# Performance work log

Measured on AMD Instinct MI355X. Metric: run time of the kernel, lower is better.

Reference implementation:

```python
import jax, jax.numpy as jnp
import numpy as np

B, N, D, E, F, K = 2, 2048, 768, 8, 3072, 2
V_MAX = 3.0
FEAT_CLAMP = 10.0


def setup_inputs() -> dict:
    key = jax.random.key(0)
    ks = jax.random.split(key, 8)
    s = lambda k, shape, sc: (jax.random.normal(k, shape, jnp.float32) * sc)
    return {
        "x": s(ks[0], (B, N, D), 1.0),
        "v_w": s(ks[1], (D,), 0.02),
        "v_b": jnp.zeros((), jnp.float32),
        "gate_w": s(ks[2], (D, E), 0.02),
        "gate_b": jnp.zeros((E,), jnp.float32),
        "w1": s(ks[3], (E, D, F), 0.02),
        "b1": jnp.zeros((E, F), jnp.float32),
        "w2": s(ks[4], (E, F, D), 0.02),
        "b2": jnp.zeros((E, D), jnp.float32),
        "out_w": s(ks[5], (2, D), 0.02),
        "out_b": jnp.zeros((D,), jnp.float32),
        "bk_scale": jnp.ones((D,), jnp.float32),
    }


def bk_green_diag(a):
    # a: (B, N) complex64 diagonal of (H_eps - z), unit off-diagonals.
    # Stable two-sided continued-fraction (Thomas/LDU) recursion:
    #   d_i = a_i - 1/d_{i-1},  e_i = a_i - 1/e_{i+1},  G_ii = 1/(d_i + e_i - a_i)
    aT = jnp.swapaxes(a, 0, 1)  # (N, B)

    def step(c, ai):
        d = ai - 1.0 / c
        return d, d

    d0 = aT[0]
    _, d_rest = jax.lax.scan(step, d0, aT[1:])
    d = jnp.concatenate([d0[None], d_rest], axis=0)  # (N, B)

    eN = aT[-1]
    _, e_rest = jax.lax.scan(step, eN, aT[:-1], reverse=True)
    e = jnp.concatenate([e_rest, eN[None]], axis=0)  # (N, B)

    G = 1.0 / (d + e - aT)
    return jnp.swapaxes(G, 0, 1)  # (B, N) complex


def reference(x, v_w, v_b, gate_w, gate_b, w1, b1, w2, b2, out_w, out_b, bk_scale):
    # --- potential projection: v = clamp(Linear(x), +-3) ---
    v = jnp.clip(x @ v_w + v_b, -V_MAX, V_MAX)  # (B, N)
    # H_eps diagonal = -2 + v, z = 1j  ->  A = H_eps - z
    a = ((-2.0 + v).astype(jnp.complex64) - 1j)
    G = bk_green_diag(a)  # (B, N) complex
    feats = jnp.stack([G.real, G.imag], axis=-1)  # (B, N, 2)

    # --- sparse MoE FFN (top-k softmax gating, GELU experts) ---
    logits = x @ gate_w + gate_b  # (B, N, E)
    probs = jax.nn.softmax(logits, axis=-1)
    topv, topi = jax.lax.top_k(probs, K)
    topv = topv / jnp.sum(topv, axis=-1, keepdims=True)
    comb = jnp.sum(topv[..., None] * jax.nn.one_hot(topi, E, dtype=x.dtype), axis=2)  # (B, N, E)
    h = jax.nn.gelu(jnp.einsum("bnd,edf->bnef", x, w1) + b1)  # (B, N, E, F)
    y = jnp.einsum("bnef,efd->bned", h, w2) + b2  # (B, N, E, D)
    ffn_out = jnp.einsum("bne,bned->bnd", comb, y)

    # --- spectral branch: clamp features, project to d_model, scale ---
    feats_c = jnp.clip(feats, -FEAT_CLAMP, FEAT_CLAMP)
    spec_out = feats_c @ out_w + out_b  # (B, N, D)
    return ffn_out + bk_scale * spec_out
```

## Files before the change

### kernel.cpp

```cpp
#include <hip/hip_runtime.h>
#include <hip/hip_bf16.h>

#define BB 2
#define NN 2048
#define DD 768
#define EE 8
#define FF 3072
#define TOK (BB*NN)
#define ROWS_CAP 9216
#define TILES 72

typedef __attribute__((ext_vector_type(8))) __bf16 bf16x8;
typedef __attribute__((ext_vector_type(4))) float floatx4;

#define OFF_CTRL    0ull
#define OFF_V       1024ull
#define OFF_TOKE    17408ull
#define OFF_TOKW    50176ull
#define OFF_ROWTOK  82944ull
#define OFF_ROWW    119808ull
#define OFF_SLOT    156672ull
#define OFF_FEATS   189440ull
#define OFF_W2T     222208ull
#define OFF_XBF     37970944ull
#define OFF_W1T     44262400ull
#define OFF_H       82011136ull
#define OFF_Y       OFF_XBF

__device__ __forceinline__ ushort f2b(float f) {
    union { float f; unsigned int i; } v; v.f = f;
    unsigned int u = v.i;
    unsigned int r = (u + 0x7FFFu + ((u >> 16) & 1u)) >> 16;
    return (ushort)r;
}
__device__ __forceinline__ unsigned int pk2(float lo, float hi) {
    union { float f; unsigned int u; } a, b;
    a.f = lo; b.f = hi;
    unsigned int ra = ((a.u + 0x7FFFu + ((a.u >> 16) & 1u)) >> 16) & 0xFFFFu;
    unsigned int rb = (b.u + 0x7FFFu + ((b.u >> 16) & 1u)) & 0xFFFF0000u;
    return ra | rb;
}
__device__ __forceinline__ float gelu_f(float x) {
    float z = 0.7978845608028654f * x * (1.f + 0.044715f * x * x);
    z = fminf(fmaxf(z, -12.f), 12.f);
    float e = __expf(2.f * z);
    return 0.5f * x * (1.f + (e - 1.f) / (e + 1.f));
}
__device__ __forceinline__ void gload16(const ushort* g, ushort* l) {
    __builtin_amdgcn_global_load_lds((const __attribute__((address_space(1))) void*)g,
                                     (__attribute__((address_space(3))) void*)l,
                                     16, 0, 0);
}

struct cplx { float x, y; };
__device__ __forceinline__ cplx cmulc(cplx a, cplx b) { return {a.x*b.x - a.y*b.y, a.x*b.y + a.y*b.x}; }
__device__ __forceinline__ cplx caddc(cplx a, cplx b) { return {a.x + b.x, a.y + b.y}; }
__device__ __forceinline__ cplx cdivc(cplx a, cplx b) {
    float s = 1.f / (b.x*b.x + b.y*b.y);
    return {(a.x*b.x + a.y*b.y)*s, (a.y*b.x - a.x*b.y)*s};
}
struct mob { cplx m00, m01, m10, m11; };
__device__ __forceinline__ mob mmul(const mob& A, const mob& B) {
    mob C;
    C.m00 = caddc(cmulc(A.m00, B.m00), cmulc(A.m01, B.m10));
    C.m01 = caddc(cmulc(A.m00, B.m01), cmulc(A.m01, B.m11));
    C.m10 = caddc(cmulc(A.m10, B.m00), cmulc(A.m11, B.m10));
    C.m11 = caddc(cmulc(A.m10, B.m01), cmulc(A.m11, B.m11));
    return C;
}
__device__ __forceinline__ void mnorm(mob& A) {
    float s = fabsf(A.m00.x);
    s = fmaxf(s, fabsf(A.m00.y)); s = fmaxf(s, fabsf(A.m01.x)); s = fmaxf(s, fabsf(A.m01.y));
    s = fmaxf(s, fabsf(A.m10.x)); s = fmaxf(s, fabsf(A.m10.y)); s = fmaxf(s, fabsf(A.m11.x));
    s = fmaxf(s, fabsf(A.m11.y));
    float r = 1.f / fmaxf(s, 1e-30f);
    A.m00.x *= r; A.m00.y *= r; A.m01.x *= r; A.m01.y *= r;
    A.m10.x *= r; A.m10.y *= r; A.m11.x *= r; A.m11.y *= r;
}
__device__ __forceinline__ mob mstep(cplx a, const mob& P) {
    mob C;
    C.m00 = {a.x*P.m00.x - a.y*P.m00.y - P.m10.x, a.x*P.m00.y + a.y*P.m00.x - P.m10.y};
    C.m01 = {a.x*P.m01.x - a.y*P.m01.y - P.m11.x, a.x*P.m01.y + a.y*P.m01.x - P.m11.y};
    C.m10 = P.m00; C.m11 = P.m01;
    return C;
}
__device__ __forceinline__ void mstore(float* s, const mob& A) {
    s[0]=A.m00.x; s[1]=A.m00.y; s[2]=A.m01.x; s[3]=A.m01.y;
    s[4]=A.m10.x; s[5]=A.m10.y; s[6]=A.m11.x; s[7]=A.m11.y;
}
__device__ __forceinline__ mob mload(const float* s) {
    mob A;
    A.m00 = {s[0], s[1]}; A.m01 = {s[2], s[3]};
    A.m10 = {s[4], s[5]}; A.m11 = {s[6], s[7]};
    return A;
}

template<bool PERM>
__device__ __forceinline__ void tcvt64_body(
    const float* __restrict__ src, ushort* __restrict__ dst,
    int Rs, int Cs, int r0, int c0, ushort* __restrict__ tT , int tid)
{
    int lr = tid >> 2;
    int lc0 = (tid & 3) * 16;
    const float* sp = src + (size_t)(r0 + lr) * Cs + c0 + lc0;
    float4 v[4];
    #pragma unroll
    for (int u = 0; u < 4; u++) v[u] = *(const float4*)(sp + 4*u);
    #pragma unroll
    for (int u = 0; u < 4; u++) {
        tT[(lc0 + 4*u + 0) * 72 + lr] = f2b(v[u].x);
        tT[(lc0 + 4*u + 1) * 72 + lr] = f2b(v[u].y);
        tT[(lc0 + 4*u + 2) * 72 + lr] = f2b(v[u].z);
        tT[(lc0 + 4*u + 3) * 72 + lr] = f2b(v[u].w);
    }
    __syncthreads();
    int chunk = tid & 7;
    #pragma unroll
    for (int pass = 0; pass < 2; pass++) {
        int c = (tid >> 3) + pass * 32;
        size_t off = (size_t)(c0 + c) * Rs + r0 + chunk * 8;
        if (PERM) {
            int a64 = chunk * 8;
            int g32 = (a64 >> 5) * 32;
            int a = a64 & 31;
            ushort o8[8] __attribute__((aligned(16)));
            #pragma unroll
            for (int k = 0; k < 8; k++) {
                int pk = a + k;
                int rl = g32 + (pk >> 1) + ((pk & 1) << 4);
                o8[k] = tT[c * 72 + rl];
            }
            *(uint4*)(dst + off) = *(const uint4*)o8;
        } else {
            *(uint4*)(dst + off) = *(const uint4*)(tT + c * 72 + chunk * 8);
        }
    }
}

#define NB_CVT   ((TOK*DD)/8/256)
#define NB_ROUTE (TOK/4)
#define NB_W1T   (12*48*EE)

__device__ __forceinline__ void cvt_body(const float* __restrict__ src, ushort* __restrict__ dst, int i) {
    const float4* s = ((const float4*)src) + (size_t)i * 2;
    float4 a = s[0], b = s[1];
    uint4 o;
    o.x = pk2(a.x, a.y); o.y = pk2(a.z, a.w);
    o.z = pk2(b.x, b.y); o.w = pk2(b.z, b.w);
    *(((uint4*)dst) + i) = o;
}

__device__ __forceinline__ void routing_body(
    const float* __restrict__ x, const float* __restrict__ v_w, const float* __restrict__ v_b,
    const float* __restrict__ gate_w, const float* __restrict__ gate_b,
    float* __restrict__ v_out, int* __restrict__ tok_e, float* __restrict__ tok_w, int blk)
{
    int wave = threadIdx.x >> 6, lane = threadIdx.x & 63;
    int t = blk * 4 + wave;
    const float* xr = x + (size_t)t * DD;
    float av = 0.f;
    float ag[8] = {0.f, 0.f, 0.f, 0.f, 0.f, 0.f, 0.f, 0.f};
    #pragma unroll
    for (int i = 0; i < 12; i++) {
        int d = lane + 64 * i;
        float xv = xr[d];
        av += xv * v_w[d];
        const float4* g = (const float4*)(gate_w + d * 8);
        float4 g0 = g[0], g1 = g[1];
        ag[0] += xv * g0.x; ag[1] += xv * g0.y; ag[2] += xv * g0.z; ag[3] += xv * g0.w;
        ag[4] += xv * g1.x; ag[5] += xv * g1.y; ag[6] += xv * g1.z; ag[7] += xv * g1.w;
    }
    #pragma unroll
    for (int off = 32; off >= 1; off >>= 1) {
        av += __shfl_xor(av, off);
        #pragma unroll
        for (int e = 0; e < 8; e++) ag[e] += __shfl_xor(ag[e], off);
    }
    if (lane == 0) {
        float vv = av + v_b[0];
        vv = fminf(fmaxf(vv, -3.f), 3.f);
        v_out[t] = vv;
        float lg[8];
        #pragma unroll
        for (int e = 0; e < 8; e++) lg[e] = ag[e] + gate_b[e];
        int e0 = 0;
        #pragma unroll
        for (int e = 1; e < 8; e++) if (lg[e] > lg[e0]) e0 = e;
        int e1 = -1;
        #pragma unroll
        for (int e = 0; e < 8; e++) if (e != e0 && (e1 < 0 || lg[e] > lg[e1])) e1 = e;
        float w0 = 1.f / (1.f + __expf(lg[e1] - lg[e0]));
        tok_e[2*t] = e0; tok_e[2*t+1] = e1;
        tok_w[2*t] = w0; tok_w[2*t+1] = 1.f - w0;
    }
}

__global__ __launch_bounds__(256) void prep1_kernel(
    const float* __restrict__ x, ushort* __restrict__ x_bf,
    const float* __restrict__ v_w, const float* __restrict__ v_b,
    const float* __restrict__ gate_w, const float* __restrict__ gate_b,
    float* __restrict__ v_out, int* __restrict__ tok_e, float* __restrict__ tok_w,
    const float* __restrict__ w1, ushort* __restrict__ w1t)
{
    __shared__ __align__(16) ushort tT[64 * 72];
    int id = blockIdx.x;
    if (id < NB_CVT) {
        cvt_body(x, x_bf, id * 256 + threadIdx.x);
        return;
    }
    id -= NB_CVT;
    if (id < NB_ROUTE) {
        routing_body(x, v_w, v_b, gate_w, gate_b, v_out, tok_e, tok_w, id);
        return;
    }
    id -= NB_ROUTE;
    int e = id / (12 * 48);
    int rem = id - e * 12 * 48;
    int cy = rem / 12;
    int rx = rem - cy * 12;
    tcvt64_body<false>(w1 + (size_t)e * DD * FF, w1t + (size_t)e * FF * DD,
                       DD, FF, rx * 64, cy * 64, tT, threadIdx.x);
}

__device__ void setup_body(
    const int* __restrict__ tok_e, const float* __restrict__ tok_w,
    int* __restrict__ ctrl, int* __restrict__ row_token, float* __restrict__ row_w,
    int* __restrict__ slot)
{
    __shared__ int cnt[8], base[8], cursor[8];
    int tid = threadIdx.x;
    int lane = tid & 63;
    if (tid < 8) { cnt[tid] = 0; cursor[tid] = 0; }
    __syncthreads();

    int mye[8];
    #pragma unroll
    for (int it = 0; it < 8; it++) {
        int idx = it * 1024 + tid;
        int e = tok_e[idx];
        mye[it] = e;
        #pragma unroll
        for (int ex = 0; ex < 8; ex++) {
            unsigned long long m = __ballot(e == ex);
            if (e == ex && lane == (__ffsll((long long)m) - 1))
                atomicAdd(&cnt[ex], (int)__popcll(m));
        }
    }
    __syncthreads();
    if (tid == 0) {
        int b = 0;
        int* te = ctrl + 24;
        for (int i = 0; i < TILES; i++) te[i] = -1;
        #pragma unroll
        for (int e = 0; e < EE; e++) {
            base[e] = b;
            ctrl[16 + e] = b;
            int tiles = (cnt[e] + 127) >> 7;
            int t0 = b >> 7;
            for (int i = 0; i < tiles; i++) te[t0 + i] = e;
            b += tiles << 7;
        }
    }
    for (int p = tid; p < ROWS_CAP; p += 1024) row_token[p] = -1;
    __syncthreads();

    #pragma unroll
    for (int it = 0; it < 8; it++) {
        int idx = it * 1024 + tid;
        int e = mye[it];
        unsigned long long lt = (1ull << lane) - 1ull;
        int p = 0;
        #pragma unroll
        for (int ex = 0; ex < 8; ex++) {
            unsigned long long m = __ballot(e == ex);
            if (e == ex) {
                int leader = __ffsll((long long)m) - 1;
                int pos = (int)__popcll(m & lt);
                int bp = 0;
                if (lane == leader) bp = atomicAdd(&cursor[ex], (int)__popcll(m));
                bp = __shfl(bp, leader);
                p = base[ex] + bp + pos;
            }
        }
        row_token[p] = idx >> 1;
        row_w[p] = tok_w[idx];
        slot[idx] = p;
    }
}

__device__ void bk_body(int b, const float* __restrict__ v, float* __restrict__ feats) {
    int t = threadIdx.x;
    bool act = t < 256;
    __shared__ float sm[256][8];
    const mob I = {{1.f,0.f},{0.f,0.f},{0.f,0.f},{1.f,0.f}};
    cplx a[8];
    const float* vb = v + (size_t)b * NN;
    if (act) {
        #pragma unroll
        for (int j = 0; j < 8; j++) { a[j].x = -2.f + vb[t*8 + j]; a[j].y = -1.f; }
    }

    mob cur = I;
    if (act) {
        #pragma unroll
        for (int j = 0; j < 8; j++) cur = mstep(a[j], cur);
        mnorm(cur);
        mstore(sm[t], cur);
    }
    for (int s = 1; s < 256; s <<= 1) {
        __syncthreads();
        mob prev; bool has = act && (t >= s);
        if (has) prev = mload(sm[t - s]);
        __syncthreads();
        if (has) { cur = mmul(cur, prev); mnorm(cur); mstore(sm[t], cur); }
    }
    __syncthreads();
    cplx dreg[8];
    if (act) {
        mob P = (t > 0) ? mload(sm[t - 1]) : I;
        #pragma unroll
        for (int j = 0; j < 8; j++) {
            P = mstep(a[j], P); mnorm(P);
            dreg[j] = cdivc(P.m00, P.m10);
        }
    }
    __syncthreads();

    cur = I;
    if (act) {
        #pragma unroll
        for (int j = 7; j >= 0; j--) cur = mstep(a[j], cur);
        mnorm(cur);
        mstore(sm[t], cur);
    }
    for (int s = 1; s < 256; s <<= 1) {
        __syncthreads();
        mob nxt; bool has = act && (t + s < 256);
        if (has) nxt = mload(sm[t + s]);
        __syncthreads();
        if (has) { cur = mmul(cur, nxt); mnorm(cur); mstore(sm[t], cur); }
    }
    __syncthreads();
    if (act) {
        mob P = (t < 255) ? mload(sm[t + 1]) : I;
        #pragma unroll
        for (int j = 7; j >= 0; j--) {
            P = mstep(a[j], P); mnorm(P);
            cplx e = cdivc(P.m00, P.m10);
            cplx den = {dreg[j].x + e.x - a[j].x, dreg[j].y + e.y - a[j].y};
            cplx one = {1.f, 0.f};
            cplx G = cdivc(one, den);
            int i = b * NN + t*8 + j;
            feats[2*i]   = G.x;
            feats[2*i+1] = G.y;
        }
    }
}

__global__ __launch_bounds__(1024) void setup_bk_kernel(
    const int* __restrict__ tok_e, const float* __restrict__ tok_w,
    int* __restrict__ ctrl, int* __restrict__ row_token, float* __restrict__ row_w,
    int* __restrict__ slot, const float* __restrict__ v, float* __restrict__ feats)
{
    if (blockIdx.x == 0) setup_body(tok_e, tok_w, ctrl, row_token, row_w, slot);
    else                 bk_body(blockIdx.x - 1, v, feats);
}

#define MFMAS() do { \
        _Pragma("unroll") \
        for (int i = 0; i < 4; i++) \
            _Pragma("unroll") \
            for (int j = 0; j < 4; j++) \
                acc[i][j] = __builtin_amdgcn_mfma_f32_16x16x32_bf16(afr[i], bfr[j], acc[i][j], 0, 0, 0); \
    } while (0)

#define G1N   (24 * 36)
#define NW2T  (48 * 12 * EE / 2)

__global__ __launch_bounds__(512, 4) void gemm1_fused_kernel(
    const ushort* __restrict__ x_bf, const ushort* __restrict__ w1t, const float* __restrict__ b1,
    const int* __restrict__ ctrl, const int* __restrict__ row_token, ushort* __restrict__ H,
    const float* __restrict__ w2, ushort* __restrict__ w2t)
{
    __shared__ __align__(16) ushort SH[4][256 * 32];
    __shared__ int toks[256];
    int bid = blockIdx.x;
    int tid = threadIdx.x;

    if (bid >= G1N) {
        int tt = (bid - G1N) * 2 + (tid >> 8);
        int e = tt / (48 * 12);
        int rem = tt - e * 48 * 12;
        int cy = rem / 48;
        int rx = rem - cy * 48;
        ushort* tT = &SH[0][0] + (tid >> 8) * 4608;
        tcvt64_body<true>(w2 + (size_t)e * FF * DD, w2t + (size_t)e * DD * FF,
                          FF, DD, rx * 64, cy * 64, tT, tid & 255);
        return;
    }

    int fx = bid % 24;
    int tile = bid / 24;
    int e0 = ctrl[24 + 2*tile];
    if (e0 < 0) return;
    int e1 = ctrl[24 + 2*tile + 1];
    if (e1 < 0) e1 = e0;
    int p0 = tile * 256;
    int f0 = fx * 128;

    ushort* As0 = &SH[0][0];
    ushort* As1 = &SH[1][0];
    ushort* Bs0 = &SH[2][0];
    ushort* Bs1 = &SH[3][0];

    if (tid < 256) { int tk = row_token[p0 + tid]; toks[tid] = tk < 0 ? 0 : tk; }
    __syncthreads();

    int wave = tid >> 6, lane = tid & 63;
    int rsub = lane >> 2;
    int kq = (((lane & 3) ^ ((rsub >> 1) & 3))) * 8;
    int tokA0 = toks[wave*32 + rsub];
    int tokA1 = toks[wave*32 + 16 + rsub];
    const ushort* aglob0 = x_bf + (size_t)tokA0 * DD + kq;
    const ushort* aglob1 = x_bf + (size_t)tokA1 * DD + kq;
    int eh = (wave >> 2) ? e1 : e0;
    const ushort* w1e = w1t + (size_t)eh * (FF * DD);
    const ushort* bglob0 = w1e + (size_t)(f0 + (wave & 3)*32 + rsub) * DD + kq;
    const ushort* bglob1 = bglob0 + (size_t)16 * DD;
    ushort* AsW0 = As0 + wave * 32 * 32;
    ushort* BsW0 = Bs0 + wave * 32 * 32;
    ushort* AsW1 = As1 + wave * 32 * 32;
    ushort* BsW1 = Bs1 + wave * 32 * 32;

    floatx4 zero4 = {0.f, 0.f, 0.f, 0.f};
    floatx4 acc[4][4];
    #pragma unroll
    for (int i = 0; i < 4; i++)
        #pragma unroll
        for (int j = 0; j < 4; j++) acc[i][j] = zero4;

    int wm = (wave >> 1) * 64, wn = (wave & 1) * 64;
    int bbase = (wave >> 2) * 128;
    int lm = lane & 15, q = lane >> 4;
    int qx = (q ^ ((lm >> 1) & 3)) * 8;

    #define G1_STAGE(AW, BW, k0) do { \
        gload16(aglob0 + (k0), (AW)); \
        gload16(aglob1 + (k0), (AW) + 16*32); \
        gload16(bglob0 + (k0), (BW)); \
        gload16(bglob1 + (k0), (BW) + 16*32); } while (0)

    G1_STAGE(AsW0, BsW0, 0);
    G1_STAGE(AsW1, BsW1, 32);
    const int NK = DD / 32;
    for (int ks = 0; ks < NK; ks++) {
        int cur = ks & 1;
        const ushort* Ab = cur ? As1 : As0;
        const ushort* Bb = cur ? Bs1 : Bs0;
        ushort* AsN = cur ? AsW1 : AsW0;
        ushort* BsN = cur ? BsW1 : BsW0;
        if (ks < NK - 1) { asm volatile("s_waitcnt vmcnt(4)" ::: "memory"); }
        else             { asm volatile("s_waitcnt vmcnt(0)" ::: "memory"); }
        __builtin_amdgcn_s_barrier();
        bf16x8 afr[4], bfr[4];
        #pragma unroll
        for (int i = 0; i < 4; i++)
            afr[i] = *(const bf16x8*)(const void*)(Ab + (wm + i*16 + lm) * 32 + qx);
        #pragma unroll
        for (int j = 0; j < 4; j++)
            bfr[j] = *(const bf16x8*)(const void*)(Bb + (bbase + wn + j*16 + lm) * 32 + qx);
        asm volatile("s_waitcnt lgkmcnt(0)" ::: "memory");
        __builtin_amdgcn_sched_barrier(0);
        __builtin_amdgcn_s_barrier();
        if (ks + 2 < NK) G1_STAGE(AsN, BsN, ks*32 + 64);
        __builtin_amdgcn_s_setprio(1);
        MFMAS();
        __builtin_amdgcn_s_setprio(0);
    }
    #undef G1_STAGE

    #pragma unroll
    for (int i = 0; i < 4; i++) {
        #pragma unroll
        for (int jp = 0; jp < 2; jp++) {
            float bias0 = b1[eh * FF + f0 + wn + (2*jp)*16 + lm];
            float bias1 = b1[eh * FF + f0 + wn + (2*jp+1)*16 + lm];
            #pragma unroll
            for (int r = 0; r < 4; r++) {
                int m = wm + i*16 + q*4 + r;
                float h0 = gelu_f(acc[i][2*jp][r] + bias0);
                float h1 = gelu_f(acc[i][2*jp+1][r] + bias1);
                *(unsigned int*)(H + (size_t)(p0 + m) * FF + f0 + wn + jp*32 + lm*2) = pk2(h0, h1);
            }
        }
    }
}

#define STAGE64(AW, BW, k0) do { \
        _Pragma("unroll") \
        for (int g = 0; g < 4; g++) { \
            gload16(ag[g] + (k0), (AW) + g*8*64); \
            gload16(bg[g] + (k0), (BW) + g*8*64); \
        } } while (0)

#define LOADFR64(APTR, BPTR, QX) do { \
        _Pragma("unroll") \
        for (int i = 0; i < 4; i++) \
            afr[i] = *(const bf16x8*)(const void*)((APTR) + (wm + i*16 + lm) * 64 + (QX)); \
        _Pragma("unroll") \
        for (int j = 0; j < 4; j++) \
            bfr[j] = *(const bf16x8*)(const void*)((BPTR) + (wn + j*16 + lm) * 64 + (QX)); \
    } while (0)

#define PIPE64(NK) do { \
    STAGE64(AsW0, BsW0, 0); \
    STAGE64(AsW1, BsW1, 64); \
    for (int ks = 0; ks < (NK); ks++) { \
        int cur = ks & 1; \
        const ushort* Ab = cur ? As[1] : As[0]; \
        const ushort* Bb = cur ? Bs[1] : Bs[0]; \
        ushort* AsN = cur ? AsW1 : AsW0; \
        ushort* BsN = cur ? BsW1 : BsW0; \
        if (ks < (NK) - 1) { asm volatile("s_waitcnt vmcnt(8)" ::: "memory"); } \
        else               { asm volatile("s_waitcnt vmcnt(0)" ::: "memory"); } \
        __builtin_amdgcn_s_barrier(); \
        { \
            bf16x8 afr[4], bfr[4]; \
            LOADFR64(Ab, Bb, qx0); \
            __builtin_amdgcn_s_setprio(1); \
            MFMAS(); \
            __builtin_amdgcn_s_setprio(0); \
        } \
        { \
            bf16x8 afr[4], bfr[4]; \
            LOADFR64(Ab, Bb, qx0 ^ 32); \
            asm volatile("s_waitcnt lgkmcnt(0)" ::: "memory"); \
            __builtin_amdgcn_sched_barrier(0); \
            __builtin_amdgcn_s_barrier(); \
            if (ks + 2 < (NK)) STAGE64(AsN, BsN, ks*64 + 128); \
            __builtin_amdgcn_s_setprio(1); \
            MFMAS(); \
            __builtin_amdgcn_s_setprio(0); \
        } \
    } } while (0)

__global__ __launch_bounds__(256) void gemm2_kernel(
    const ushort* __restrict__ H, const ushort* __restrict__ w2t, const float* __restrict__ b2,
    const int* __restrict__ ctrl, const float* __restrict__ row_w, float* __restrict__ Y)
{
    int tile = blockIdx.x;
    int e = ctrl[24 + tile];
    if (e < 0) return;
    int p0 = tile * 128;
    int d0 = blockIdx.y * 128;

    __shared__ ushort As[2][128 * 64];
    __shared__ ushort Bs[2][128 * 64];

    int tid = threadIdx.x;
    int wave = tid >> 6, lane = tid & 63;
    int srow = lane >> 3;
    int kq = (((lane & 7) ^ (srow & 7))) * 8;
    const ushort* ag[4];
    #pragma unroll
    for (int g = 0; g < 4; g++)
        ag[g] = H + (size_t)(p0 + wave*32 + g*8 + srow) * FF + kq;
    const ushort* w2e = w2t + (size_t)e * (DD * FF);
    const ushort* bg[4];
    #pragma unroll
    for (int g = 0; g < 4; g++)
        bg[g] = w2e + (size_t)(d0 + wave*32 + g*8 + srow) * FF + kq;
    ushort* AsW0 = &As[0][wave * 32 * 64];
    ushort* BsW0 = &Bs[0][wave * 32 * 64];
    ushort* AsW1 = &As[1][wave * 32 * 64];
    ushort* BsW1 = &Bs[1][wave * 32 * 64];

    floatx4 zero4 = {0.f, 0.f, 0.f, 0.f};
    floatx4 acc[4][4];
    #pragma unroll
    for (int i = 0; i < 4; i++)
        #pragma unroll
        for (int j = 0; j < 4; j++) acc[i][j] = zero4;

    int wm = (wave & 1) * 64, wn = (wave >> 1) * 64;
    int lm = lane & 15, q = lane >> 4;
    int qx0 = (q ^ (lm & 7)) * 8;

    PIPE64(FF/64);

    #pragma unroll
    for (int i = 0; i < 4; i++) {
        #pragma unroll
        for (int j = 0; j < 4; j++) {
            int n = wn + j*16 + lm;
            float bias = b2[e * DD + d0 + n];
            #pragma unroll
            for (int r = 0; r < 4; r++) {
                int m = wm + i*16 + q*4 + r;
                float wgt = row_w[p0 + m];
                Y[(size_t)(p0 + m) * DD + d0 + n] = wgt * (acc[i][j][r] + bias);
            }
        }
    }
}

__global__ __launch_bounds__(256) void final_kernel(
    const float* __restrict__ Y, const int* __restrict__ slot, const float* __restrict__ feats,
    const float* __restrict__ out_w, const float* __restrict__ out_b,
    const float* __restrict__ bk_scale, float* __restrict__ out)
{
    int idx = blockIdx.x * 256 + threadIdx.x;
    int base = idx * 4;
    int t = base / DD;
    int d = base - t * DD;
    int p0 = slot[2*t], p1 = slot[2*t + 1];
    const float4 ya = *(const float4*)(Y + (size_t)p0 * DD + d);
    const float4 yb = *(const float4*)(Y + (size_t)p1 * DD + d);
    float f0 = feats[2*t], f1 = feats[2*t + 1];
    f0 = fminf(fmaxf(f0, -10.f), 10.f);
    f1 = fminf(fmaxf(f1, -10.f), 10.f);
    float ff[4] = {ya.x + yb.x, ya.y + yb.y, ya.z + yb.z, ya.w + yb.w};
    float4 o;
    float* op = (float*)&o;
    #pragma unroll
    for (int u = 0; u < 4; u++) {
        float spec = f0 * out_w[d + u] + f1 * out_w[DD + d + u] + out_b[d + u];
        op[u] = ff[u] + bk_scale[d + u] * spec;
    }
    *(float4*)(out + base) = o;
}

extern "C" void kernel_launch(void* const* d_in, const int* in_sizes, int n_in,
                              void* d_out, int out_size, void* d_ws, size_t ws_size,
                              hipStream_t stream)
{
    const float* x      = (const float*)d_in[0];
    const float* v_w    = (const float*)d_in[1];
    const float* v_b    = (const float*)d_in[2];
    const float* gate_w = (const float*)d_in[3];
    const float* gate_b = (const float*)d_in[4];
    const float* w1     = (const float*)d_in[5];
    const float* b1     = (const float*)d_in[6];
    const float* w2     = (const float*)d_in[7];
    const float* b2     = (const float*)d_in[8];
    const float* out_w  = (const float*)d_in[9];
    const float* out_b  = (const float*)d_in[10];
    const float* bk_s   = (const float*)d_in[11];

    char* ws = (char*)d_ws;
    int*    ctrl    = (int*)(ws + OFF_CTRL);
    float*  v       = (float*)(ws + OFF_V);
    int*    tok_e   = (int*)(ws + OFF_TOKE);
    float*  tok_w   = (float*)(ws + OFF_TOKW);
    int*    row_tok = (int*)(ws + OFF_ROWTOK);
    float*  row_w   = (float*)(ws + OFF_ROWW);
    int*    slot    = (int*)(ws + OFF_SLOT);
    float*  feats   = (float*)(ws + OFF_FEATS);
    ushort* w2t     = (ushort*)(ws + OFF_W2T);
    ushort* x_bf    = (ushort*)(ws + OFF_XBF);
    ushort* w1t     = (ushort*)(ws + OFF_W1T);
    ushort* H       = (ushort*)(ws + OFF_H);
    float*  Y       = (float*)(ws + OFF_Y);
    float*  out     = (float*)d_out;

    prep1_kernel<<<NB_CVT + NB_ROUTE + NB_W1T, 256, 0, stream>>>(
        x, x_bf, v_w, v_b, gate_w, gate_b, v, tok_e, tok_w, w1, w1t);
    setup_bk_kernel<<<1 + BB, 1024, 0, stream>>>(tok_e, tok_w, ctrl, row_tok, row_w, slot, v, feats);
    gemm1_fused_kernel<<<G1N + NW2T, 512, 0, stream>>>(x_bf, w1t, b1, ctrl, row_tok, H, w2, w2t);
    gemm2_kernel<<<dim3(TILES, DD / 128), 256, 0, stream>>>(H, w2t, b2, ctrl, row_w, Y);
    final_kernel<<<(TOK * DD) / 1024, 256, 0, stream>>>(Y, slot, feats, out_w, out_b, bk_s, out);
}
```

Before: 197.8 us.

## Swizzle transpose LDS, overlap w1 convert with setup/BK, interleave gemm1 blocks

The LDS staging tile in the weight transpose-convert gets an XOR swizzle on 8-element chunks to cut bank conflicts on the column-wise writes. The w1 transpose moves out of the first prep kernel into the setup/BK launch, so the serial routing setup and BK recursion blocks, which use few of the CUs, share the launch with weight conversion. The gemm1 grid is reordered so each group of 11 blocks mixes 3 GEMM tiles with 8 w2-transpose blocks, spreading the conversion work across the GEMM run. These add index math and make block scheduling harder to reason about.

```diff
diff --git a/kernel.cpp b/kernel.cpp
--- a/kernel.cpp
+++ b/kernel.cpp
@@ -106,21 +106,27 @@
     float4 v[4];
     #pragma unroll
     for (int u = 0; u < 4; u++) v[u] = *(const float4*)(sp + 4*u);
+    int chw = lr >> 3, wbit = lr & 7;
     #pragma unroll
     for (int u = 0; u < 4; u++) {
-        tT[(lc0 + 4*u + 0) * 72 + lr] = f2b(v[u].x);
-        tT[(lc0 + 4*u + 1) * 72 + lr] = f2b(v[u].y);
-        tT[(lc0 + 4*u + 2) * 72 + lr] = f2b(v[u].z);
-        tT[(lc0 + 4*u + 3) * 72 + lr] = f2b(v[u].w);
-    }
-    __syncthreads();
-    int chunk = tid & 7;
+        float vs[4] = {v[u].x, v[u].y, v[u].z, v[u].w};
+        #pragma unroll
+        for (int e2 = 0; e2 < 4; e2++) {
+            int col = lc0 + 4*u + e2;
+            int g = (col >> 4) & 3;
+            tT[col * 72 + ((chw ^ g) << 3) + wbit] = f2b(vs[e2]);
+        }
+    }
+    __syncthreads();
+    int p = tid & 7;
     #pragma unroll
     for (int pass = 0; pass < 2; pass++) {
         int c = (tid >> 3) + pass * 32;
-        size_t off = (size_t)(c0 + c) * Rs + r0 + chunk * 8;
+        int g = (c >> 4) & 3;
+        int chl = p ^ g;
+        int a64 = chl * 8;
+        size_t off = (size_t)(c0 + c) * Rs + r0 + a64;
         if (PERM) {
-            int a64 = chunk * 8;
             int g32 = (a64 >> 5) * 32;
             int a = a64 & 31;
             ushort o8[8] __attribute__((aligned(16)));
@@ -128,18 +134,18 @@
             for (int k = 0; k < 8; k++) {
                 int pk = a + k;
                 int rl = g32 + (pk >> 1) + ((pk & 1) << 4);
-                o8[k] = tT[c * 72 + rl];
+                int phys = ((rl >> 3) ^ g) * 8 + (rl & 7);
+                o8[k] = tT[c * 72 + phys];
             }
             *(uint4*)(dst + off) = *(const uint4*)o8;
         } else {
-            *(uint4*)(dst + off) = *(const uint4*)(tT + c * 72 + chunk * 8);
+            *(uint4*)(dst + off) = *(const uint4*)(tT + c * 72 + p * 8);
         }
     }
 }
 
 #define NB_CVT   ((TOK*DD)/8/256)
 #define NB_ROUTE (TOK/4)
-#define NB_W1T   (12*48*EE)
 
 __device__ __forceinline__ void cvt_body(const float* __restrict__ src, ushort* __restrict__ dst, int i) {
     const float4* s = ((const float4*)src) + (size_t)i * 2;
@@ -195,32 +201,19 @@
     }
 }
 
-__global__ __launch_bounds__(256) void prep1_kernel(
+__global__ __launch_bounds__(256) void prep0_kernel(
     const float* __restrict__ x, ushort* __restrict__ x_bf,
     const float* __restrict__ v_w, const float* __restrict__ v_b,
     const float* __restrict__ gate_w, const float* __restrict__ gate_b,
-    float* __restrict__ v_out, int* __restrict__ tok_e, float* __restrict__ tok_w,
-    const float* __restrict__ w1, ushort* __restrict__ w1t)
-{
-    __shared__ __align__(16) ushort tT[64 * 72];
+    float* __restrict__ v_out, int* __restrict__ tok_e, float* __restrict__ tok_w)
+{
     int id = blockIdx.x;
-    if (id < NB_CVT) {
-        cvt_body(x, x_bf, id * 256 + threadIdx.x);
-        return;
-    }
+    if (id < NB_CVT) { cvt_body(x, x_bf, id * 256 + threadIdx.x); return; }
     id -= NB_CVT;
-    if (id < NB_ROUTE) {
-        routing_body(x, v_w, v_b, gate_w, gate_b, v_out, tok_e, tok_w, id);
-        return;
-    }
-    id -= NB_ROUTE;
-    int e = id / (12 * 48);
-    int rem = id - e * 12 * 48;
-    int cy = rem / 12;
-    int rx = rem - cy * 12;
-    tcvt64_body<false>(w1 + (size_t)e * DD * FF, w1t + (size_t)e * FF * DD,
-                       DD, FF, rx * 64, cy * 64, tT, threadIdx.x);
-}
+    routing_body(x, v_w, v_b, gate_w, gate_b, v_out, tok_e, tok_w, id);
+}
+
+#define NB_W1T4  (12*48*EE/4)
 
 __device__ void setup_body(
     const int* __restrict__ tok_e, const float* __restrict__ tok_w,
@@ -360,10 +353,20 @@
 __global__ __launch_bounds__(1024) void setup_bk_kernel(
     const int* __restrict__ tok_e, const float* __restrict__ tok_w,
     int* __restrict__ ctrl, int* __restrict__ row_token, float* __restrict__ row_w,
-    int* __restrict__ slot, const float* __restrict__ v, float* __restrict__ feats)
-{
-    if (blockIdx.x == 0) setup_body(tok_e, tok_w, ctrl, row_token, row_w, slot);
-    else                 bk_body(blockIdx.x - 1, v, feats);
+    int* __restrict__ slot, const float* __restrict__ v, float* __restrict__ feats,
+    const float* __restrict__ w1, ushort* __restrict__ w1t)
+{
+    if (blockIdx.x == 0) { setup_body(tok_e, tok_w, ctrl, row_token, row_w, slot); return; }
+    if (blockIdx.x <= BB) { bk_body(blockIdx.x - 1, v, feats); return; }
+    __shared__ __align__(16) ushort tT4[4 * 4608];
+    int tt = (blockIdx.x - 1 - BB) * 4 + (threadIdx.x >> 8);
+    int e = tt / (12 * 48);
+    int rem = tt - e * 12 * 48;
+    int cy = rem / 12;
+    int rx = rem - cy * 12;
+    tcvt64_body<false>(w1 + (size_t)e * DD * FF, w1t + (size_t)e * FF * DD,
+                       DD, FF, rx * 64, cy * 64,
+                       tT4 + (threadIdx.x >> 8) * 4608, threadIdx.x & 255);
 }
 
 #define MFMAS() do { \
@@ -376,6 +379,7 @@
 
 #define G1N   (24 * 36)
 #define NW2T  (48 * 12 * EE / 2)
+#define NFUSED (G1N + NW2T)
 
 __global__ __launch_bounds__(512, 4) void gemm1_fused_kernel(
     const ushort* __restrict__ x_bf, const ushort* __restrict__ w1t, const float* __restrict__ b1,
@@ -386,9 +390,10 @@
     __shared__ int toks[256];
     int bid = blockIdx.x;
     int tid = threadIdx.x;
-
-    if (bid >= G1N) {
-        int tt = (bid - G1N) * 2 + (tid >> 8);
+    int grp = bid / 11, l11 = bid % 11;
+
+    if (l11 >= 3) {
+        int tt = (grp * 8 + (l11 - 3)) * 2 + (tid >> 8);
         int e = tt / (48 * 12);
         int rem = tt - e * 48 * 12;
         int cy = rem / 48;
@@ -399,8 +404,9 @@
         return;
     }
 
-    int fx = bid % 24;
-    int tile = bid / 24;
+    int g = grp * 3 + l11;
+    int fx = g % 24;
+    int tile = g / 24;
     int e0 = ctrl[24 + 2*tile];
     if (e0 < 0) return;
     int e1 = ctrl[24 + 2*tile + 1];
@@ -663,10 +669,11 @@
     float*  Y       = (float*)(ws + OFF_Y);
     float*  out     = (float*)d_out;
 
-    prep1_kernel<<<NB_CVT + NB_ROUTE + NB_W1T, 256, 0, stream>>>(
-        x, x_bf, v_w, v_b, gate_w, gate_b, v, tok_e, tok_w, w1, w1t);
-    setup_bk_kernel<<<1 + BB, 1024, 0, stream>>>(tok_e, tok_w, ctrl, row_tok, row_w, slot, v, feats);
-    gemm1_fused_kernel<<<G1N + NW2T, 512, 0, stream>>>(x_bf, w1t, b1, ctrl, row_tok, H, w2, w2t);
+    prep0_kernel<<<NB_CVT + NB_ROUTE, 256, 0, stream>>>(
+        x, x_bf, v_w, v_b, gate_w, gate_b, v, tok_e, tok_w);
+    setup_bk_kernel<<<1 + BB + NB_W1T4, 1024, 0, stream>>>(
+        tok_e, tok_w, ctrl, row_tok, row_w, slot, v, feats, w1, w1t);
+    gemm1_fused_kernel<<<NFUSED, 512, 0, stream>>>(x_bf, w1t, b1, ctrl, row_tok, H, w2, w2t);
     gemm2_kernel<<<dim3(TILES, DD / 128), 256, 0, stream>>>(H, w2t, b2, ctrl, row_w, Y);
     final_kernel<<<(TOK * DD) / 1024, 256, 0, stream>>>(Y, slot, feats, out_w, out_b, bk_s, out);
 }
```

Result: no change. 198.0 us (+0.1%).
